# Kernel optimization log

Hardware: AMD Instinct MI355X
Metric: run time of the kernel (lower is better)

The kernel has to match this reference:

```python
import math
import jax, jax.numpy as jnp
import numpy as np

B, S, D = 1, 1024, 2048
E, TOPK, H, DK, CONV = 8, 2, 6, 256, 4
DV = 2 * DK            # expand_v = 2
KD, VD = H * DK, H * DV
EPS = 1e-5
CAP_LEN = math.ceil(S * TOPK / TOPK * 1.0)  # capacity = 1.0 -> S


def setup_inputs() -> dict:
    key = jax.random.key(0)
    ks = jax.random.split(key, 16)
    sd = 0.02
    dt = jnp.exp(jax.random.uniform(ks[8], (H,)) * (math.log(0.1) - math.log(0.001)) + math.log(0.001))
    dt = jnp.clip(dt, 1e-4, None)
    dt_bias = dt + jnp.log(-jnp.expm1(-dt))
    return {
        'hidden_states': jax.random.normal(ks[0], (B, S, D), jnp.float32),
        'q_w': jax.random.normal(ks[1], (D, KD), jnp.float32) * sd,
        'gate_w': jax.random.normal(ks[2], (D, E), jnp.float32) * sd,
        'k_w': jax.random.normal(ks[3], (E, D, KD), jnp.float32) * sd,
        'v_w': jax.random.normal(ks[4], (E, D, VD), jnp.float32) * sd,
        'b_w': jax.random.normal(ks[5], (E, D, H), jnp.float32) * sd,
        'a_w': jax.random.normal(ks[6], (E, D, H), jnp.float32) * sd,
        'A_log': jnp.log(jax.random.uniform(ks[7], (H,), minval=1e-2, maxval=16.0)),
        'dt_bias': dt_bias,
        'q_conv_w': jax.random.normal(ks[9], (KD, CONV), jnp.float32) * 0.1,
        'k_conv_w': jax.random.normal(ks[10], (KD, CONV), jnp.float32) * 0.1,
        'v_conv_w': jax.random.normal(ks[11], (VD, CONV), jnp.float32) * 0.1,
        'g_w': jax.random.normal(ks[12], (D, VD), jnp.float32) * sd,
        'norm_w': jnp.ones((DV,), jnp.float32),
        'o_w': jax.random.normal(ks[13], (VD, D), jnp.float32) * sd,
    }


def _short_conv(x, w):
    # depthwise causal conv1d + silu. x: (N,T,C), w: (C,K)
    N, T, C = x.shape
    K = w.shape[1]
    y = jax.lax.conv_general_dilated(x.transpose(0, 2, 1), w[:, None, :], (1,),
                                     [(K - 1, 0)], feature_group_count=C)
    return jax.nn.silu(y.transpose(0, 2, 1))


def _l2norm(x):
    return x * jax.lax.rsqrt((x * x).sum(-1, keepdims=True) + 1e-6)


def reference(hidden_states, q_w, gate_w, k_w, v_w, b_w, a_w, A_log, dt_bias,
              q_conv_w, k_conv_w, v_conv_w, g_w, norm_w, o_w):
    b, s, d = B, S, D
    s_exp = s * TOPK
    # ---- router: softmax -> topk -> renormalize ----
    probs = jax.nn.softmax(hidden_states @ gate_w, axis=-1)        # (b,s,E)
    rw, sel = jax.lax.top_k(probs, TOPK)                           # (b,s,K)
    rw = rw / rw.sum(-1, keepdims=True)
    routing_mask = jax.nn.one_hot(sel, E, dtype=jnp.int32).sum(2)  # (b,s,E)
    # ---- transform(): dispatch tokens into per-expert capacity buffers ----
    x_rep = jnp.repeat(hidden_states, TOPK, axis=1)                # (b,s*K,d)
    sel_flat = sel.reshape(-1)
    batch_idx = jnp.repeat(jnp.arange(b), s_exp)
    sorted_indices = jnp.argsort(batch_idx * E + sel_flat)         # stable sort keeps temporal order
    x_sorted = x_rep.reshape(-1, d)[sorted_indices]
    counts = routing_mask.sum(1)                                   # (b,E) tokens per (batch,expert)
    flat_off = (jnp.cumsum(counts, 1) + (jnp.arange(b) * s_exp)[:, None]).reshape(-1)
    starts = jnp.concatenate([jnp.zeros((1,), flat_off.dtype), flat_off[:-1]])
    idx = jnp.arange(CAP_LEN)[None, :] + starts[:, None]
    trunc = idx + counts.reshape(-1)[:, None] - CAP_LEN            # right-align, drop overflow
    valid = (trunc < flat_off[:, None]) & (trunc >= 0) & (trunc >= starts[:, None])
    trunc = jnp.where(valid, trunc, 0)                             # (b*E, CAP_LEN)
    xe = x_sorted[trunc.reshape(-1)] * valid.reshape(-1)[:, None]
    xe = xe.reshape(b, E, CAP_LEN, d).transpose(1, 0, 2, 3)        # (E,b,T,d)
    T = CAP_LEN
    # ---- per-expert projections ----
    q = jnp.einsum('ebtd,dk->ebtk', xe, q_w)
    k = jnp.einsum('ebtd,edk->ebtk', xe, k_w)
    v = jnp.einsum('ebtd,edk->ebtk', xe, v_w)
    beta = jax.nn.sigmoid(jnp.einsum('ebtd,edh->ebth', xe, b_w))
    g = -jnp.exp(A_log) * jax.nn.softplus(jnp.einsum('ebtd,edh->ebth', xe, a_w) + dt_bias)
    # ---- short conv + silu, head split, qk l2 norm ----
    N = E * b
    q = _short_conv(q.reshape(N, T, KD), q_conv_w).reshape(N, T, H, DK)
    k = _short_conv(k.reshape(N, T, KD), k_conv_w).reshape(N, T, H, DK)
    v = _short_conv(v.reshape(N, T, VD), v_conv_w).reshape(N, T, H, DV)
    q = _l2norm(q) * (DK ** -0.5)
    k = _l2norm(k)
    beta = beta.reshape(N, T, H)
    g = g.reshape(N, T, H)
    # ---- gated delta rule recurrence: S_t = a_t S + beta_t k_t (v_t - a_t S^T k_t)^T ----
    def step(Sst, inp):
        q_t, k_t, v_t, b_t, g_t = inp
        Sst = Sst * jnp.exp(g_t)[..., None, None]
        pred = jnp.einsum('nhk,nhkv->nhv', k_t, Sst)
        delta = (v_t - pred) * b_t[..., None]
        Sst = Sst + jnp.einsum('nhk,nhv->nhkv', k_t, delta)
        o_t = jnp.einsum('nhk,nhkv->nhv', q_t, Sst)
        return Sst, o_t
    xs = (q.transpose(1, 0, 2, 3), k.transpose(1, 0, 2, 3), v.transpose(1, 0, 2, 3),
          beta.transpose(1, 0, 2), g.transpose(1, 0, 2))
    S0 = jnp.zeros((N, H, DK, DV), q.dtype)
    _, o = jax.lax.scan(step, S0, xs)                              # (T,N,H,DV)
    o = o.transpose(1, 0, 2, 3).reshape(E, b, T, H, DV)
    # ---- reconstruct(): scatter back and combine with routing weights ----
    re = o.transpose(1, 0, 2, 3, 4).reshape(b * E * T, H, DV)
    re = re * valid.reshape(-1)[:, None, None]
    resorted = jnp.zeros((b * s_exp, H, DV), re.dtype).at[trunc.reshape(-1)].add(re)
    restored = resorted[jnp.argsort(sorted_indices)].reshape(b, s, TOPK, H, DV)
    o_comb = (restored * rw[..., None, None]).sum(2)               # (b,s,H,DV)
    # ---- gated RMSNorm (swish gate) + output projection ----
    gg = (hidden_states @ g_w).reshape(b, s, H, DV)
    rms = o_comb * jax.lax.rsqrt((o_comb * o_comb).mean(-1, keepdims=True) + EPS)
    o_out = rms * norm_w * (gg * jax.nn.sigmoid(gg))
    return o_out.reshape(b, s, VD) @ o_w
```

## Files before the change

kernel.cpp:

```cpp
#include <hip/hip_runtime.h>
#include <math.h>

#define Dm    2048
#define Hh    6
#define DKk   256
#define DVv   512
#define KD    1536
#define VD    3072
#define CH    4

typedef __attribute__((ext_vector_type(8))) __bf16 bf16x8;
typedef __attribute__((ext_vector_type(4))) float floatx4;

__device__ __forceinline__ unsigned short f2bf(float f) {
    unsigned int u = __float_as_uint(f);
    u = (u + 0x7fffu + ((u >> 16) & 1u)) >> 16;
    return (unsigned short)u;
}

__device__ __forceinline__ void gl_lds16(const void* g, void* l) {
    __builtin_amdgcn_global_load_lds((const __attribute__((address_space(1))) void*)g,
                                     (__attribute__((address_space(3))) void*)l, 16, 0, 0);
}

__global__ void router_kernel(const float* __restrict__ hidden,
                              const float* __restrict__ gate_w,
                              int* __restrict__ sel01, float* __restrict__ w01)
{
    int t = blockIdx.x;
    int lane = threadIdx.x;
    const float* hr = hidden + (size_t)t * Dm;
    float h[32];
#pragma unroll
    for (int i = 0; i < 32; ++i) h[i] = hr[lane + 64 * i];
    float logit[8];
#pragma unroll
    for (int e = 0; e < 8; ++e) {
        float acc = 0.f;
#pragma unroll
        for (int i = 0; i < 32; ++i) acc += h[i] * gate_w[(size_t)(lane + 64 * i) * 8 + e];
#pragma unroll
        for (int off = 1; off < 64; off <<= 1) acc += __shfl_xor(acc, off, 64);
        logit[e] = acc;
    }
    if (lane == 0) {
        int i0 = 0;
#pragma unroll
        for (int e = 1; e < 8; ++e) if (logit[e] > logit[i0]) i0 = e;
        int i1 = (i0 == 0) ? 1 : 0;
#pragma unroll
        for (int e = 0; e < 8; ++e) if (e != i0 && logit[e] > logit[i1]) i1 = e;
        float w0 = 1.f / (1.f + expf(logit[i1] - logit[i0]));
        sel01[2 * t] = i0; sel01[2 * t + 1] = i1;
        w01[2 * t] = w0;   w01[2 * t + 1] = 1.f - w0;
    }
}

__global__ void dispatch_kernel(const int* __restrict__ sel01,
                                int* __restrict__ list_c, int* __restrict__ posg,
                                int* __restrict__ cnt, int* __restrict__ basearr)
{
    __shared__ int wbase[16];
    __shared__ int sbase;
    int t = threadIdx.x;
    int lane = t & 63, w = t >> 6;
    int s0 = sel01[2 * t], s1 = sel01[2 * t + 1];
    if (t == 0) sbase = 0;
    __syncthreads();
    for (int e = 0; e < 8; ++e) {
        int flag  = (s0 == e || s1 == e) ? 1 : 0;
        int kslot = (s0 == e) ? 0 : 1;
        unsigned long long m = __ballot(flag);
        int lpre = __popcll(m & ((1ull << lane) - 1ull));
        if (lane == 0) wbase[w] = __popcll(m);
        __syncthreads();
        if (t == 0) {
            int run = sbase;
            basearr[e] = run;
            for (int i = 0; i < 16; ++i) { int tv = wbase[i]; wbase[i] = run; run += tv; }
            cnt[e] = run - sbase;
            sbase = run;
        }
        __syncthreads();
        if (flag) {
            int pos = wbase[w] + lpre;
            list_c[pos] = t;
            posg[2 * t + kslot] = pos;
        }
        __syncthreads();
    }
}

__global__ void cast_bf16_kernel(const float* __restrict__ x, unsigned short* __restrict__ y)
{
    int i = (blockIdx.x * 256 + threadIdx.x) * 4;
    float4 a = *(const float4*)(x + i);
    ushort4 o;
    o.x = f2bf(a.x); o.y = f2bf(a.y); o.z = f2bf(a.z); o.w = f2bf(a.w);
    *(ushort4*)(y + i) = o;
}

__global__ void gather_cast_kernel(const float* __restrict__ hidden, const int* __restrict__ list,
                                   unsigned short* __restrict__ xe)
{
    int slot = blockIdx.x;
    int tok = list[slot];
    const float* src = hidden + (size_t)tok * Dm;
    unsigned short* dst = xe + (size_t)slot * Dm;
    int c = threadIdx.x * 8;
    float4 a = *(const float4*)(src + c);
    float4 b = *(const float4*)(src + c + 4);
    ushort4 o1, o2;
    o1.x = f2bf(a.x); o1.y = f2bf(a.y); o1.z = f2bf(a.z); o1.w = f2bf(a.w);
    o2.x = f2bf(b.x); o2.y = f2bf(b.y); o2.z = f2bf(b.z); o2.w = f2bf(b.w);
    *(ushort4*)(dst + c) = o1;
    *(ushort4*)(dst + c + 4) = o2;
}

__global__ void transpose_cast_kernel(const float* __restrict__ in, unsigned short* __restrict__ out,
                                      int K, int N)
{
    __shared__ float tile[32][33];
    int b = blockIdx.z;
    int k0 = blockIdx.x * 32, n0 = blockIdx.y * 32;
    const float* ip = in + (size_t)b * K * N;
    unsigned short* op = out + (size_t)b * K * N;
    int tx = threadIdx.x & 31, ty = threadIdx.x >> 5;
#pragma unroll
    for (int i = 0; i < 4; ++i)
        tile[ty + i * 8][tx] = ip[(size_t)(k0 + ty + i * 8) * N + n0 + tx];
    __syncthreads();
#pragma unroll
    for (int i = 0; i < 4; ++i)
        op[(size_t)(n0 + ty + i * 8) * K + k0 + tx] = f2bf(tile[tx][ty + i * 8]);
}

template<bool EXPERT>
__global__ __launch_bounds__(256)
void gemm_bf16(const unsigned short* __restrict__ A,
               const unsigned short* __restrict__ Bt,
               float* __restrict__ C,
               const int* __restrict__ cnt, const int* __restrict__ basearr,
               int M, int K, int N)
{
    int e = EXPERT ? blockIdx.z : 0;
    int Mloc = M, base = 0;
    if (EXPERT) {
        Mloc = cnt[e]; base = basearr[e];
        if ((int)(blockIdx.x * 128) >= Mloc) return;
    }
    int m0 = blockIdx.x * 128, n0 = blockIdx.y * 128;
    const unsigned short* Ab = A + (size_t)base * K;
    const unsigned short* Bb = Bt + (size_t)e * (size_t)K * N;
    __shared__ unsigned short As[4][128 * 32];
    __shared__ unsigned short Bs[4][128 * 32];
    int tid = threadIdx.x;
    int lane = tid & 63, wave = tid >> 6;
    const unsigned short* ga[2];
    const unsigned short* gb[2];
    int lo[2];
#pragma unroll
    for (int j = 0; j < 2; ++j) {
        int flat = j * 256 + tid;
        int row = flat >> 2, sub = flat & 3;
        int ar = m0 + row; if (ar > Mloc - 1) ar = Mloc - 1;
        ga[j] = Ab + (size_t)ar * K + sub * 8;
        gb[j] = Bb + (size_t)(n0 + row) * K + sub * 8;
        lo[j] = flat * 8;
    }
    floatx4 acc[4][4];
#pragma unroll
    for (int i = 0; i < 4; ++i)
#pragma unroll
        for (int j = 0; j < 4; ++j) acc[i][j] = (floatx4){0.f, 0.f, 0.f, 0.f};

    int wm = (wave >> 1) * 64, wn = (wave & 1) * 64;
    int fr = lane & 15, kr = (lane >> 4) * 8;

    int nk = K >> 5;
    auto stage = [&](int buf, int t) {
        int k0 = t << 5;
        gl_lds16(ga[0] + k0, As[buf] + lo[0]);
        gl_lds16(gb[0] + k0, Bs[buf] + lo[0]);
        gl_lds16(ga[1] + k0, As[buf] + lo[1]);
        gl_lds16(gb[1] + k0, Bs[buf] + lo[1]);
    };
    stage(0, 0);
    stage(1, 1);
    stage(2, 2);
    int cur = 0;
    for (int t = 0; t < nk; ++t) {
        int nxt = (cur + 3) & 3;
        if (t + 3 < nk) stage(nxt, t + 3);
        int ahead = nk - 1 - t;
        if (ahead >= 3)      asm volatile("s_waitcnt vmcnt(12)\n\ts_barrier" ::: "memory");
        else if (ahead == 2) asm volatile("s_waitcnt vmcnt(8)\n\ts_barrier" ::: "memory");
        else if (ahead == 1) asm volatile("s_waitcnt vmcnt(4)\n\ts_barrier" ::: "memory");
        else                 asm volatile("s_waitcnt vmcnt(0)\n\ts_barrier" ::: "memory");
        bf16x8 af[4], bfr[4];
        const unsigned short* Ac = As[cur];
        const unsigned short* Bc = Bs[cur];
#pragma unroll
        for (int f = 0; f < 4; ++f) {
            af[f]  = *(const bf16x8*)(Ac + (size_t)(wm + f * 16 + fr) * 32 + kr);
            bfr[f] = *(const bf16x8*)(Bc + (size_t)(wn + f * 16 + fr) * 32 + kr);
        }
#pragma unroll
        for (int fm = 0; fm < 4; ++fm)
#pragma unroll
            for (int fn = 0; fn < 4; ++fn)
                acc[fm][fn] = __builtin_amdgcn_mfma_f32_16x16x32_bf16(af[fm], bfr[fn], acc[fm][fn], 0, 0, 0);
        asm volatile("s_waitcnt lgkmcnt(0)\n\ts_barrier" ::: "memory");
        cur = (cur + 1) & 3;
    }
    int rb = (lane >> 4) * 4;
#pragma unroll
    for (int fm = 0; fm < 4; ++fm) {
#pragma unroll
        for (int r = 0; r < 4; ++r) {
            int m = m0 + wm + fm * 16 + rb + r;
            if (m < Mloc) {
                float* cp = C + (size_t)(base + m) * N + n0 + wn + fr;
#pragma unroll
                for (int fn = 0; fn < 4; ++fn)
                    cp[fn * 16] = acc[fm][fn][r];
            }
        }
    }
}

__global__ void ba_kernel(const float* __restrict__ hidden,
                          const float* __restrict__ b_w, const float* __restrict__ a_w,
                          const float* __restrict__ A_log, const float* __restrict__ dt_bias,
                          const int* __restrict__ list, const int* __restrict__ cnt,
                          const int* __restrict__ basearr,
                          float* __restrict__ beta_c, float* __restrict__ g_c)
{
    int j = blockIdx.x, e = blockIdx.y;
    if (j >= cnt[e]) return;
    int gpos = basearr[e] + j;
    int tok = list[gpos];
    int lane = threadIdx.x;
    const float* hr = hidden + (size_t)tok * Dm;
    float h[32];
#pragma unroll
    for (int i = 0; i < 32; ++i) h[i] = hr[lane + 64 * i];
    for (int c = 0; c < 12; ++c) {
        int col = c % 6;
        const float* W = ((c < 6) ? b_w : a_w) + (size_t)e * Dm * 6;
        float acc = 0.f;
#pragma unroll
        for (int i = 0; i < 32; ++i) acc += h[i] * W[(size_t)(lane + 64 * i) * 6 + col];
#pragma unroll
        for (int off = 1; off < 64; off <<= 1) acc += __shfl_xor(acc, off, 64);
        if (lane == 0) {
            if (c < 6) {
                beta_c[gpos * 6 + col] = 1.f / (1.f + expf(-acc));
            } else {
                float x = acc + dt_bias[col];
                float sp = (x > 20.f) ? x : log1pf(expf(x));
                g_c[gpos * 6 + col] = -expf(A_log[col]) * sp;
            }
        }
    }
}

template<bool GATHER>
__global__ void conv_norm_kernel(const float* __restrict__ X,
                                 const float* __restrict__ convw,
                                 const int* __restrict__ list, const int* __restrict__ cnt,
                                 const int* __restrict__ basearr,
                                 float* __restrict__ outb, float scale)
{
    int j = blockIdx.x, e = blockIdx.y, h = blockIdx.z;
    if (j >= cnt[e]) return;
    int base = basearr[e];
    int gpos = base + j;
    int c = h * DKk + threadIdx.x;
    float acc = 0.f;
#pragma unroll
    for (int tau = 0; tau < 4; ++tau) {
        int jj = j - 3 + tau;
        if (jj >= 0) {
            const float* row = GATHER ? (X + (size_t)list[base + jj] * KD)
                                      : (X + (size_t)(base + jj) * KD);
            acc += row[c] * convw[c * 4 + tau];
        }
    }
    float y = acc / (1.f + expf(-acc));
    float v = y * y;
#pragma unroll
    for (int off = 1; off < 64; off <<= 1) v += __shfl_xor(v, off, 64);
    __shared__ float red[4];
    if ((threadIdx.x & 63) == 0) red[threadIdx.x >> 6] = v;
    __syncthreads();
    float total = red[0] + red[1] + red[2] + red[3];
    outb[(size_t)gpos * KD + c] = y * rsqrtf(total + 1e-6f) * scale;
}

__global__ void conv_v_kernel(const float* __restrict__ X,
                              const float* __restrict__ convw,
                              const int* __restrict__ cnt, const int* __restrict__ basearr,
                              float* __restrict__ outb)
{
    int j = blockIdx.x, e = blockIdx.y;
    if (j >= cnt[e]) return;
    int base = basearr[e];
    int gpos = base + j;
    int c = blockIdx.z * 256 + threadIdx.x;
    float acc = 0.f;
#pragma unroll
    for (int tau = 0; tau < 4; ++tau) {
        int jj = j - 3 + tau;
        if (jj >= 0) acc += X[(size_t)(base + jj) * VD + c] * convw[c * 4 + tau];
    }
    outb[(size_t)gpos * VD + c] = acc / (1.f + expf(-acc));
}

__global__ void qk_kernel(const float* __restrict__ qn, const float* __restrict__ kn,
                          float* __restrict__ qk_c)
{
    int gpos = blockIdx.x, h = blockIdx.y;
    int lane = threadIdx.x;
    const float4* qp = (const float4*)(qn + (size_t)gpos * KD + h * DKk);
    const float4* kp = (const float4*)(kn + (size_t)gpos * KD + h * DKk);
    float4 a = qp[lane], b = kp[lane];
    float acc = a.x * b.x + a.y * b.y + a.z * b.z + a.w * b.w;
#pragma unroll
    for (int off = 1; off < 64; off <<= 1) acc += __shfl_xor(acc, off, 64);
    if (lane == 0) qk_c[(size_t)gpos * Hh + h] = acc;
}

__global__ __launch_bounds__(256, 3)
void recurrence_kernel(const float* __restrict__ qn, const float* __restrict__ kn,
                       const float* __restrict__ vc,
                       const float* __restrict__ beta_c, const float* __restrict__ g_c,
                       const float* __restrict__ qk_c,
                       const int* __restrict__ cnt, const int* __restrict__ basearr,
                       float* __restrict__ o_c)
{
    int vb = blockIdx.x, h = blockIdx.y, e = blockIdx.z;
    int n = cnt[e], base = basearr[e];
    if (n <= 0) return;
    int tid = threadIdx.x;
    int kpart = tid & 7, vcol = tid >> 3;
    int v = vb * 32 + vcol;
    int wv = tid >> 6, lane = tid & 63;

    __shared__ float lk[2][CH][256];
    __shared__ float lq[2][CH][256];

    const float* kb = kn + (size_t)base * KD + h * DKk;
    const float* qb = qn + (size_t)base * KD + h * DKk;
    const float* vp = vc + (size_t)base * VD + h * DVv + v;
    const float* gp = g_c    + (size_t)base * Hh + h;
    const float* bp = beta_c + (size_t)base * Hh + h;
    const float* xp = qk_c   + (size_t)base * Hh + h;
    float* op = o_c + (size_t)base * VD + h * DVv + v;

    float4 s[8];
#pragma unroll
    for (int i = 0; i < 8; ++i) s[i] = make_float4(0.f, 0.f, 0.f, 0.f);

    int nch = (n + CH - 1) / CH;

    auto stageKQ = [&](int buf, int c) {
        int jj = c * CH + wv; if (jj > n - 1) jj = n - 1;
        gl_lds16(kb + (size_t)jj * KD + lane * 4, &lk[buf][wv][lane * 4]);
        gl_lds16(qb + (size_t)jj * KD + lane * 4, &lq[buf][wv][lane * 4]);
    };

    float vA[CH], gA[CH], bA[CH], xA[CH];
    float vB[CH], gB[CH], bB[CH], xB[CH];

    auto loadScal = [&](float (&V)[CH], float (&G)[CH], float (&B)[CH], float (&X)[CH], int c) {
#pragma unroll
        for (int u = 0; u < CH; ++u) {
            int jj = c * CH + u; if (jj > n - 1) jj = n - 1;
            V[u] = vp[(size_t)jj * VD];
            G[u] = gp[(size_t)jj * Hh];
            B[u] = bp[(size_t)jj * Hh];
            X[u] = xp[(size_t)jj * Hh];
        }
    };

    auto computeChunk = [&](const float (&Lk)[CH][256], const float (&Lq)[CH][256],
                            const float (&V)[CH], const float (&G)[CH],
                            const float (&B)[CH], const float (&X)[CH], int c) {
#pragma unroll
        for (int u = 0; u < CH; ++u) {
            const float* Lku = &Lk[u][kpart * 4];
            const float* Lqu = &Lq[u][kpart * 4];
            float4 pa0 = make_float4(0.f,0.f,0.f,0.f), pa1 = make_float4(0.f,0.f,0.f,0.f);
            float4 ra0 = make_float4(0.f,0.f,0.f,0.f), ra1 = make_float4(0.f,0.f,0.f,0.f);
            float4 kk[8];
#pragma unroll
            for (int i = 0; i < 8; ++i) {
                kk[i] = *(const float4*)(Lku + i * 32);
                float4 qq = *(const float4*)(Lqu + i * 32);
                float4& pa = (i & 1) ? pa1 : pa0;
                float4& ra = (i & 1) ? ra1 : ra0;
                pa.x = fmaf(kk[i].x, s[i].x, pa.x); pa.y = fmaf(kk[i].y, s[i].y, pa.y);
                pa.z = fmaf(kk[i].z, s[i].z, pa.z); pa.w = fmaf(kk[i].w, s[i].w, pa.w);
                ra.x = fmaf(qq.x, s[i].x, ra.x); ra.y = fmaf(qq.y, s[i].y, ra.y);
                ra.z = fmaf(qq.z, s[i].z, ra.z); ra.w = fmaf(qq.w, s[i].w, ra.w);
            }
            float p = ((pa0.x + pa1.x) + (pa0.y + pa1.y)) + ((pa0.z + pa1.z) + (pa0.w + pa1.w));
            float r = ((ra0.x + ra1.x) + (ra0.y + ra1.y)) + ((ra0.z + ra1.z) + (ra0.w + ra1.w));
#pragma unroll
            for (int m = 1; m < 8; m <<= 1) {
                p += __shfl_xor(p, m, 64);
                r += __shfl_xor(r, m, 64);
            }
            float eg = __expf(G[u]);
            float delta = (V[u] - p * eg) * B[u];
            float out = fmaf(X[u], delta, eg * r);
#pragma unroll
            for (int i = 0; i < 8; ++i) {
                s[i].x = fmaf(eg, s[i].x, kk[i].x * delta);
                s[i].y = fmaf(eg, s[i].y, kk[i].y * delta);
                s[i].z = fmaf(eg, s[i].z, kk[i].z * delta);
                s[i].w = fmaf(eg, s[i].w, kk[i].w * delta);
            }
            int j = c * CH + u;
            if (kpart == 0 && j < n) op[(size_t)j * VD] = out;
        }
    };

    stageKQ(0, 0);
    loadScal(vA, gA, bA, xA, 0);
    stageKQ(1, 1);
    asm volatile("s_waitcnt vmcnt(2)\n\ts_barrier" ::: "memory");

    for (int c = 0; c < nch; c += 2) {
        loadScal(vB, gB, bB, xB, c + 1);
        computeChunk(lk[0], lq[0], vA, gA, bA, xA, c);
        __syncthreads();
        stageKQ(0, c + 2);
        asm volatile("s_waitcnt vmcnt(2)\n\ts_barrier" ::: "memory");
        if (c + 1 >= nch) break;
        loadScal(vA, gA, bA, xA, c + 2);
        computeChunk(lk[1], lq[1], vB, gB, bB, xB, c + 1);
        __syncthreads();
        stageKQ(1, c + 3);
        asm volatile("s_waitcnt vmcnt(2)\n\ts_barrier" ::: "memory");
    }
    asm volatile("s_waitcnt vmcnt(0)" ::: "memory");
}

__global__ void combine_kernel(const float* __restrict__ o_c, const float* __restrict__ gg,
                               const float* __restrict__ norm_w,
                               const int* __restrict__ posg, const float* __restrict__ w01,
                               unsigned short* __restrict__ ocg)
{
    int t = blockIdx.x, h = blockIdx.y;
    int p0 = posg[2 * t], p1 = posg[2 * t + 1];
    float w0 = w01[2 * t], w1 = w01[2 * t + 1];
    int v0 = threadIdx.x, v1 = threadIdx.x + 256;
    size_t r0 = (size_t)p0 * VD + h * DVv, r1 = (size_t)p1 * VD + h * DVv;
    float a  = w0 * o_c[r0 + v0] + w1 * o_c[r1 + v0];
    float b2 = w0 * o_c[r0 + v1] + w1 * o_c[r1 + v1];
    float val = a * a + b2 * b2;
#pragma unroll
    for (int off = 1; off < 64; off <<= 1) val += __shfl_xor(val, off, 64);
    __shared__ float red[4];
    if ((threadIdx.x & 63) == 0) red[threadIdx.x >> 6] = val;
    __syncthreads();
    float total = red[0] + red[1] + red[2] + red[3];
    float rms = rsqrtf(total / 512.f + 1e-5f);
    size_t og = (size_t)t * VD + h * DVv;
    float g0 = gg[og + v0], g1 = gg[og + v1];
    ocg[og + v0] = f2bf(a  * rms * norm_w[v0] * g0 / (1.f + expf(-g0)));
    ocg[og + v1] = f2bf(b2 * rms * norm_w[v1] * g1 / (1.f + expf(-g1)));
}

extern "C" void kernel_launch(void* const* d_in, const int* in_sizes, int n_in,
                              void* d_out, int out_size, void* d_ws, size_t ws_size,
                              hipStream_t stream)
{
    const float* hidden   = (const float*)d_in[0];
    const float* q_w      = (const float*)d_in[1];
    const float* gate_w   = (const float*)d_in[2];
    const float* k_w      = (const float*)d_in[3];
    const float* v_w      = (const float*)d_in[4];
    const float* b_w      = (const float*)d_in[5];
    const float* a_w      = (const float*)d_in[6];
    const float* A_log    = (const float*)d_in[7];
    const float* dt_bias  = (const float*)d_in[8];
    const float* q_conv_w = (const float*)d_in[9];
    const float* k_conv_w = (const float*)d_in[10];
    const float* v_conv_w = (const float*)d_in[11];
    const float* g_w      = (const float*)d_in[12];
    const float* norm_w   = (const float*)d_in[13];
    const float* o_w      = (const float*)d_in[14];
    float* outp = (float*)d_out;

    float* f = (float*)d_ws;
    size_t off = 0;
    auto alloc = [&](size_t n) { float* p = f + off; off += (n + 3) & ~(size_t)3; return p; };
    float* qh     = alloc((size_t)1024 * 1536);
    float* kraw   = alloc((size_t)2048 * 1536);
    float* qn     = alloc((size_t)2048 * 1536);
    float* kn     = alloc((size_t)2048 * 1536);
    float* vraw   = alloc((size_t)2048 * 3072);
    float* vconv  = alloc((size_t)2048 * 3072);
    float* gg     = alloc((size_t)1024 * 3072);
    float* beta_c = alloc(2048 * 6);
    float* g_c    = alloc(2048 * 6);
    float* qk_c   = alloc(2048 * 6);
    float* w01f   = alloc(2048);

    unsigned short* u = (unsigned short*)(f + off);
    size_t uoff = 0;
    auto ualloc = [&](size_t n) { unsigned short* p = u + uoff; uoff += (n + 7) & ~(size_t)7; return p; };
    unsigned short* hidden_bf = ualloc((size_t)1024 * 2048);
    unsigned short* xe_c      = ualloc((size_t)2048 * 2048);
    unsigned short* ocg       = ualloc((size_t)1024 * 3072);
    unsigned short* q_wT      = ualloc((size_t)2048 * 1536);
    unsigned short* k_wT      = ualloc((size_t)8 * 2048 * 1536);
    unsigned short* v_wT      = ualloc((size_t)8 * 2048 * 3072);
    unsigned short* g_wT      = ualloc((size_t)2048 * 3072);
    unsigned short* o_wT      = ualloc((size_t)3072 * 2048);

    int* ib      = (int*)(u + uoff);
    int* sel01   = ib;
    int* list_c  = ib + 2048;
    int* posg    = ib + 4096;
    int* cnt     = ib + 6144;
    int* basearr = ib + 6152;
    float* o_c = vraw;

    router_kernel<<<1024, 64, 0, stream>>>(hidden, gate_w, sel01, w01f);
    dispatch_kernel<<<1, 1024, 0, stream>>>(sel01, list_c, posg, cnt, basearr);

    cast_bf16_kernel<<<2048, 256, 0, stream>>>(hidden, hidden_bf);
    gather_cast_kernel<<<2048, 256, 0, stream>>>(hidden, list_c, xe_c);
    transpose_cast_kernel<<<dim3(64, 48, 1), 256, 0, stream>>>(q_w, q_wT, 2048, 1536);
    transpose_cast_kernel<<<dim3(64, 48, 8), 256, 0, stream>>>(k_w, k_wT, 2048, 1536);
    transpose_cast_kernel<<<dim3(64, 96, 8), 256, 0, stream>>>(v_w, v_wT, 2048, 3072);
    transpose_cast_kernel<<<dim3(64, 96, 1), 256, 0, stream>>>(g_w, g_wT, 2048, 3072);
    transpose_cast_kernel<<<dim3(96, 64, 1), 256, 0, stream>>>(o_w, o_wT, 3072, 2048);

    gemm_bf16<false><<<dim3(8, 12), 256, 0, stream>>>(hidden_bf, q_wT, qh, nullptr, nullptr, 1024, 2048, 1536);
    gemm_bf16<true ><<<dim3(8, 12, 8), 256, 0, stream>>>(xe_c, k_wT, kraw, cnt, basearr, 0, 2048, 1536);
    gemm_bf16<true ><<<dim3(8, 24, 8), 256, 0, stream>>>(xe_c, v_wT, vraw, cnt, basearr, 0, 2048, 3072);
    gemm_bf16<false><<<dim3(8, 24), 256, 0, stream>>>(hidden_bf, g_wT, gg, nullptr, nullptr, 1024, 2048, 3072);

    ba_kernel<<<dim3(1024, 8), 64, 0, stream>>>(hidden, b_w, a_w, A_log, dt_bias,
                                                list_c, cnt, basearr, beta_c, g_c);

    conv_norm_kernel<true ><<<dim3(1024, 8, 6), 256, 0, stream>>>(qh,   q_conv_w, list_c, cnt, basearr, qn, 0.0625f);
    conv_norm_kernel<false><<<dim3(1024, 8, 6), 256, 0, stream>>>(kraw, k_conv_w, list_c, cnt, basearr, kn, 1.0f);
    conv_v_kernel<<<dim3(1024, 8, 12), 256, 0, stream>>>(vraw, v_conv_w, cnt, basearr, vconv);

    qk_kernel<<<dim3(2048, 6), 64, 0, stream>>>(qn, kn, qk_c);

    recurrence_kernel<<<dim3(16, 6, 8), 256, 0, stream>>>(qn, kn, vconv, beta_c, g_c, qk_c,
                                                          cnt, basearr, o_c);

    combine_kernel<<<dim3(1024, 6), 256, 0, stream>>>(o_c, gg, norm_w, posg, w01f, ocg);
    gemm_bf16<false><<<dim3(8, 16), 256, 0, stream>>>(ocg, o_wT, outp, nullptr, nullptr, 1024, 3072, 2048);
}
```

Before: 1.286 ms.

## Merge q/g and k/v projection GEMMs and split recurrence state across more blocks

The q and g weight matrices are transposed into one concatenated weight, and the same is done for the per-expert k and v weights. This turns four GEMM launches into two wider ones whose outputs share a row stride of 4608, and the conv and combine kernels now read through that stride. Separately, the recurrence kernel splits each value column's key dimension over 16 threads instead of 8 and launches twice as many blocks, halving per-thread state registers and allowing more blocks per CU. The trade-offs are one extra shuffle stage per step in the recurrence and larger merged buffers.

Result: slower. 1.347 ms (+4.7%).

```diff
diff --git a/kernel.cpp b/kernel.cpp
--- a/kernel.cpp
+++ b/kernel.cpp
@@ -7,6 +7,7 @@
 #define DVv   512
 #define KD    1536
 #define VD    3072
+#define QGW   4608
 #define CH    4
 
 typedef __attribute__((ext_vector_type(8))) __bf16 bf16x8;
@@ -118,13 +119,13 @@
 }
 
 __global__ void transpose_cast_kernel(const float* __restrict__ in, unsigned short* __restrict__ out,
-                                      int K, int N)
+                                      int K, int N, size_t estride)
 {
     __shared__ float tile[32][33];
     int b = blockIdx.z;
     int k0 = blockIdx.x * 32, n0 = blockIdx.y * 32;
     const float* ip = in + (size_t)b * K * N;
-    unsigned short* op = out + (size_t)b * K * N;
+    unsigned short* op = out + (size_t)b * estride;
     int tx = threadIdx.x & 31, ty = threadIdx.x >> 5;
 #pragma unroll
     for (int i = 0; i < 4; ++i)
@@ -266,7 +267,7 @@
 }
 
 template<bool GATHER>
-__global__ void conv_norm_kernel(const float* __restrict__ X,
+__global__ void conv_norm_kernel(const float* __restrict__ X, int xstride,
                                  const float* __restrict__ convw,
                                  const int* __restrict__ list, const int* __restrict__ cnt,
                                  const int* __restrict__ basearr,
@@ -282,8 +283,8 @@
     for (int tau = 0; tau < 4; ++tau) {
         int jj = j - 3 + tau;
         if (jj >= 0) {
-            const float* row = GATHER ? (X + (size_t)list[base + jj] * KD)
-                                      : (X + (size_t)(base + jj) * KD);
+            const float* row = GATHER ? (X + (size_t)list[base + jj] * xstride)
+                                      : (X + (size_t)(base + jj) * xstride);
             acc += row[c] * convw[c * 4 + tau];
         }
     }
@@ -312,7 +313,7 @@
 #pragma unroll
     for (int tau = 0; tau < 4; ++tau) {
         int jj = j - 3 + tau;
-        if (jj >= 0) acc += X[(size_t)(base + jj) * VD + c] * convw[c * 4 + tau];
+        if (jj >= 0) acc += X[(size_t)(base + jj) * QGW + KD + c] * convw[c * 4 + tau];
     }
     outb[(size_t)gpos * VD + c] = acc / (1.f + expf(-acc));
 }
@@ -331,7 +332,7 @@
     if (lane == 0) qk_c[(size_t)gpos * Hh + h] = acc;
 }
 
-__global__ __launch_bounds__(256, 3)
+__global__ __launch_bounds__(256, 4)
 void recurrence_kernel(const float* __restrict__ qn, const float* __restrict__ kn,
                        const float* __restrict__ vc,
                        const float* __restrict__ beta_c, const float* __restrict__ g_c,
@@ -343,8 +344,8 @@
     int n = cnt[e], base = basearr[e];
     if (n <= 0) return;
     int tid = threadIdx.x;
-    int kpart = tid & 7, vcol = tid >> 3;
-    int v = vb * 32 + vcol;
+    int kpart = tid & 15, vcol = tid >> 4;
+    int v = vb * 16 + vcol;
     int wv = tid >> 6, lane = tid & 63;
 
     __shared__ float lk[2][CH][256];
@@ -358,9 +359,9 @@
     const float* xp = qk_c   + (size_t)base * Hh + h;
     float* op = o_c + (size_t)base * VD + h * DVv + v;
 
-    float4 s[8];
-#pragma unroll
-    for (int i = 0; i < 8; ++i) s[i] = make_float4(0.f, 0.f, 0.f, 0.f);
+    float4 s[4];
+#pragma unroll
+    for (int i = 0; i < 4; ++i) s[i] = make_float4(0.f, 0.f, 0.f, 0.f);
 
     int nch = (n + CH - 1) / CH;
 
@@ -393,11 +394,11 @@
             const float* Lqu = &Lq[u][kpart * 4];
             float4 pa0 = make_float4(0.f,0.f,0.f,0.f), pa1 = make_float4(0.f,0.f,0.f,0.f);
             float4 ra0 = make_float4(0.f,0.f,0.f,0.f), ra1 = make_float4(0.f,0.f,0.f,0.f);
-            float4 kk[8];
-#pragma unroll
-            for (int i = 0; i < 8; ++i) {
-                kk[i] = *(const float4*)(Lku + i * 32);
-                float4 qq = *(const float4*)(Lqu + i * 32);
+            float4 kk[4];
+#pragma unroll
+            for (int i = 0; i < 4; ++i) {
+                kk[i] = *(const float4*)(Lku + i * 64);
+                float4 qq = *(const float4*)(Lqu + i * 64);
                 float4& pa = (i & 1) ? pa1 : pa0;
                 float4& ra = (i & 1) ? ra1 : ra0;
                 pa.x = fmaf(kk[i].x, s[i].x, pa.x); pa.y = fmaf(kk[i].y, s[i].y, pa.y);
@@ -408,7 +409,7 @@
             float p = ((pa0.x + pa1.x) + (pa0.y + pa1.y)) + ((pa0.z + pa1.z) + (pa0.w + pa1.w));
             float r = ((ra0.x + ra1.x) + (ra0.y + ra1.y)) + ((ra0.z + ra1.z) + (ra0.w + ra1.w));
 #pragma unroll
-            for (int m = 1; m < 8; m <<= 1) {
+            for (int m = 1; m < 16; m <<= 1) {
                 p += __shfl_xor(p, m, 64);
                 r += __shfl_xor(r, m, 64);
             }
@@ -416,7 +417,7 @@
             float delta = (V[u] - p * eg) * B[u];
             float out = fmaf(X[u], delta, eg * r);
 #pragma unroll
-            for (int i = 0; i < 8; ++i) {
+            for (int i = 0; i < 4; ++i) {
                 s[i].x = fmaf(eg, s[i].x, kk[i].x * delta);
                 s[i].y = fmaf(eg, s[i].y, kk[i].y * delta);
                 s[i].z = fmaf(eg, s[i].z, kk[i].z * delta);
@@ -448,7 +449,7 @@
     asm volatile("s_waitcnt vmcnt(0)" ::: "memory");
 }
 
-__global__ void combine_kernel(const float* __restrict__ o_c, const float* __restrict__ gg,
+__global__ void combine_kernel(const float* __restrict__ o_c, const float* __restrict__ qg,
                                const float* __restrict__ norm_w,
                                const int* __restrict__ posg, const float* __restrict__ w01,
                                unsigned short* __restrict__ ocg)
@@ -469,7 +470,8 @@
     float total = red[0] + red[1] + red[2] + red[3];
     float rms = rsqrtf(total / 512.f + 1e-5f);
     size_t og = (size_t)t * VD + h * DVv;
-    float g0 = gg[og + v0], g1 = gg[og + v1];
+    size_t gq = (size_t)t * QGW + KD + h * DVv;
+    float g0 = qg[gq + v0], g1 = qg[gq + v1];
     ocg[og + v0] = f2bf(a  * rms * norm_w[v0] * g0 / (1.f + expf(-g0)));
     ocg[og + v1] = f2bf(b2 * rms * norm_w[v1] * g1 / (1.f + expf(-g1)));
 }
@@ -498,13 +500,12 @@
     float* f = (float*)d_ws;
     size_t off = 0;
     auto alloc = [&](size_t n) { float* p = f + off; off += (n + 3) & ~(size_t)3; return p; };
-    float* qh     = alloc((size_t)1024 * 1536);
-    float* kraw   = alloc((size_t)2048 * 1536);
+    float* qg     = alloc((size_t)1024 * QGW);
+    float* kvraw  = alloc((size_t)2048 * QGW);
     float* qn     = alloc((size_t)2048 * 1536);
     float* kn     = alloc((size_t)2048 * 1536);
-    float* vraw   = alloc((size_t)2048 * 3072);
     float* vconv  = alloc((size_t)2048 * 3072);
-    float* gg     = alloc((size_t)1024 * 3072);
+    float* o_c    = alloc((size_t)2048 * 3072);
     float* beta_c = alloc(2048 * 6);
     float* g_c    = alloc(2048 * 6);
     float* qk_c   = alloc(2048 * 6);
@@ -516,10 +517,8 @@
     unsigned short* hidden_bf = ualloc((size_t)1024 * 2048);
     unsigned short* xe_c      = ualloc((size_t)2048 * 2048);
     unsigned short* ocg       = ualloc((size_t)1024 * 3072);
-    unsigned short* q_wT      = ualloc((size_t)2048 * 1536);
-    unsigned short* k_wT      = ualloc((size_t)8 * 2048 * 1536);
-    unsigned short* v_wT      = ualloc((size_t)8 * 2048 * 3072);
-    unsigned short* g_wT      = ualloc((size_t)2048 * 3072);
+    unsigned short* qg_wT     = ualloc((size_t)QGW * 2048);
+    unsigned short* kv_wT     = ualloc((size_t)8 * QGW * 2048);
     unsigned short* o_wT      = ualloc((size_t)3072 * 2048);
 
     int* ib      = (int*)(u + uoff);
@@ -528,36 +527,35 @@
     int* posg    = ib + 4096;
     int* cnt     = ib + 6144;
     int* basearr = ib + 6152;
-    float* o_c = vraw;
+
+    const size_t EST = (size_t)2048 * QGW;
 
     router_kernel<<<1024, 64, 0, stream>>>(hidden, gate_w, sel01, w01f);
     dispatch_kernel<<<1, 1024, 0, stream>>>(sel01, list_c, posg, cnt, basearr);
 
     cast_bf16_kernel<<<2048, 256, 0, stream>>>(hidden, hidden_bf);
     gather_cast_kernel<<<2048, 256, 0, stream>>>(hidden, list_c, xe_c);
-    transpose_cast_kernel<<<dim3(64, 48, 1), 256, 0, stream>>>(q_w, q_wT, 2048, 1536);
-    transpose_cast_kernel<<<dim3(64, 48, 8), 256, 0, stream>>>(k_w, k_wT, 2048, 1536);
-    transpose_cast_kernel<<<dim3(64, 96, 8), 256, 0, stream>>>(v_w, v_wT, 2048, 3072);
-    transpose_cast_kernel<<<dim3(64, 96, 1), 256, 0, stream>>>(g_w, g_wT, 2048, 3072);
-    transpose_cast_kernel<<<dim3(96, 64, 1), 256, 0, stream>>>(o_w, o_wT, 3072, 2048);
-
-    gemm_bf16<false><<<dim3(8, 12), 256, 0, stream>>>(hidden_bf, q_wT, qh, nullptr, nullptr, 1024, 2048, 1536);
-    gemm_bf16<true ><<<dim3(8, 12, 8), 256, 0, stream>>>(xe_c, k_wT, kraw, cnt, basearr, 0, 2048, 1536);
-    gemm_bf16<true ><<<dim3(8, 24, 8), 256, 0, stream>>>(xe_c, v_wT, vraw, cnt, basearr, 0, 2048, 3072);
-    gemm_bf16<false><<<dim3(8, 24), 256, 0, stream>>>(hidden_bf, g_wT, gg, nullptr, nullptr, 1024, 2048, 3072);
+    transpose_cast_kernel<<<dim3(64, 48, 1), 256, 0, stream>>>(q_w, qg_wT, 2048, 1536, 0);
+    transpose_cast_kernel<<<dim3(64, 96, 1), 256, 0, stream>>>(g_w, qg_wT + (size_t)1536 * 2048, 2048, 3072, 0);
+    transpose_cast_kernel<<<dim3(64, 48, 8), 256, 0, stream>>>(k_w, kv_wT, 2048, 1536, EST);
+    transpose_cast_kernel<<<dim3(64, 96, 8), 256, 0, stream>>>(v_w, kv_wT + (size_t)1536 * 2048, 2048, 3072, EST);
+    transpose_cast_kernel<<<dim3(96, 64, 1), 256, 0, stream>>>(o_w, o_wT, 3072, 2048, 0);
+
+    gemm_bf16<false><<<dim3(8, 36), 256, 0, stream>>>(hidden_bf, qg_wT, qg, nullptr, nullptr, 1024, 2048, QGW);
+    gemm_bf16<true ><<<dim3(8, 36, 8), 256, 0, stream>>>(xe_c, kv_wT, kvraw, cnt, basearr, 0, 2048, QGW);
 
     ba_kernel<<<dim3(1024, 8), 64, 0, stream>>>(hidden, b_w, a_w, A_log, dt_bias,
                                                 list_c, cnt, basearr, beta_c, g_c);
 
-    conv_norm_kernel<true ><<<dim3(1024, 8, 6), 256, 0, stream>>>(qh,   q_conv_w, list_c, cnt, basearr, qn, 0.0625f);
-    conv_norm_kernel<false><<<dim3(1024, 8, 6), 256, 0, stream>>>(kraw, k_conv_w, list_c, cnt, basearr, kn, 1.0f);
-    conv_v_kernel<<<dim3(1024, 8, 12), 256, 0, stream>>>(vraw, v_conv_w, cnt, basearr, vconv);
+    conv_norm_kernel<true ><<<dim3(1024, 8, 6), 256, 0, stream>>>(qg,    QGW, q_conv_w, list_c, cnt, basearr, qn, 0.0625f);
+    conv_norm_kernel<false><<<dim3(1024, 8, 6), 256, 0, stream>>>(kvraw, QGW, k_conv_w, list_c, cnt, basearr, kn, 1.0f);
+    conv_v_kernel<<<dim3(1024, 8, 12), 256, 0, stream>>>(kvraw, v_conv_w, cnt, basearr, vconv);
 
     qk_kernel<<<dim3(2048, 6), 64, 0, stream>>>(qn, kn, qk_c);
 
-    recurrence_kernel<<<dim3(16, 6, 8), 256, 0, stream>>>(qn, kn, vconv, beta_c, g_c, qk_c,
+    recurrence_kernel<<<dim3(32, 6, 8), 256, 0, stream>>>(qn, kn, vconv, beta_c, g_c, qk_c,
                                                           cnt, basearr, o_c);
 
-    combine_kernel<<<dim3(1024, 6), 256, 0, stream>>>(o_c, gg, norm_w, posg, w01f, ocg);
+    combine_kernel<<<dim3(1024, 6), 256, 0, stream>>>(o_c, qg, norm_w, posg, w01f, ocg);
     gemm_bf16<false><<<dim3(8, 16), 256, 0, stream>>>(ocg, o_wT, outp, nullptr, nullptr, 1024, 3072, 2048);
 }
```
